# Kernel optimization log

Hardware: AMD Instinct MI355X
Metric: run time of the kernel (lower is better)

The kernel has to match this reference:

```python
import jax, jax.numpy as jnp
import numpy as np

# Layer node counts: [n0, n1, n2, n3] for a 3-hop sampled subgraph
N_NODES = [524288, 65536, 8192, 1024]
DIMS = [100, 256, 256, 47]


def sage_conv(x_src, x_dst, src, dst, Wl, bl, Wr, n_dst):
    # PyG SAGEConv: lin_l(mean_agg(neighbors)) + lin_r(root)
    msg = x_src[src]                                        # [E, in]
    agg = jax.ops.segment_sum(msg, dst, num_segments=n_dst)  # [n_dst, in]
    cnt = jax.ops.segment_sum(jnp.ones((src.shape[0],), dtype=x_src.dtype), dst,
                              num_segments=n_dst)
    agg = agg / jnp.maximum(cnt, 1.0)[:, None]               # mean, 0-deg -> 0
    return agg @ Wl + bl + x_dst @ Wr


def setup_inputs() -> dict:
    key = jax.random.key(0)
    ks = jax.random.split(key, 20)
    inp = {"x": jax.random.normal(ks[0], (N_NODES[0], DIMS[0]), dtype=jnp.float32)}
    E = [655360, 81920, 10240]
    for i in range(3):
        inp[f"src{i}"] = jax.random.randint(ks[1 + 2 * i], (E[i],), 0, N_NODES[i])
        inp[f"dst{i}"] = jax.random.randint(ks[2 + 2 * i], (E[i],), 0, N_NODES[i + 1])
    for i in range(3):
        fin, fout = DIMS[i], DIMS[i + 1]
        inp[f"Wl{i}"] = jax.random.normal(ks[7 + 3 * i], (fin, fout), jnp.float32) * (1.0 / np.sqrt(fin))
        inp[f"bl{i}"] = jnp.zeros((fout,), jnp.float32)
        inp[f"Wr{i}"] = jax.random.normal(ks[8 + 3 * i], (fin, fout), jnp.float32) * (1.0 / np.sqrt(fin))
    return inp


def reference(x, src0, dst0, src1, dst1, src2, dst2,
              Wl0, bl0, Wr0, Wl1, bl1, Wr1, Wl2, bl2, Wr2):
    srcs = [src0, src1, src2]
    dsts = [dst0, dst1, dst2]
    Wls = [Wl0, Wl1, Wl2]
    bls = [bl0, bl1, bl2]
    Wrs = [Wr0, Wr1, Wr2]
    h = x
    for i in range(3):
        n_dst = N_NODES[i + 1]
        h_dst = h[:n_dst]
        h = sage_conv(h, h_dst, srcs[i], dsts[i], Wls[i], bls[i], Wrs[i], n_dst)
        if i != 2:
            h = jax.nn.relu(h)  # dropout is identity in eval mode
    return jax.nn.log_softmax(h, axis=-1)
```

## Files before the change

### kernel.cpp

```cpp
#include <hip/hip_runtime.h>
#include <math.h>

constexpr int NN1 = 65536, NN2 = 8192, NN3 = 1024;
constexpr int E0 = 655360, E1 = 81920, E2 = 10240;
constexpr int ETOT = E0 + E1 + E2;
constexpr int NTOT = NN1 + NN2 + NN3;

static inline int cdiv(int a, int b) { return (a + b - 1) / b; }

typedef __bf16 bf16x8_t __attribute__((ext_vector_type(8)));
typedef float f32x4_t __attribute__((ext_vector_type(4)));

__device__ __forceinline__ unsigned short f2bf(float f) {
    union { float f; unsigned int u; } v; v.f = f;
    unsigned int r = v.u + 0x7fffu + ((v.u >> 16) & 1u);
    return (unsigned short)(r >> 16);
}
__device__ __forceinline__ float bf2f(unsigned short h) {
    union { unsigned int u; float f; } v; v.u = ((unsigned int)h) << 16;
    return v.f;
}

__global__ void count_all(const int* __restrict__ dst0, const int* __restrict__ dst1,
                          const int* __restrict__ dst2, int* __restrict__ cnt) {
    int i = blockIdx.x * 256 + threadIdx.x;
    if (i < E0) atomicAdd(&cnt[dst0[i]], 1);
    else if (i < E0 + E1) atomicAdd(&cnt[NN1 + dst1[i - E0]], 1);
    else if (i < ETOT) atomicAdd(&cnt[NN1 + NN2 + dst2[i - E0 - E1]], 1);
}

__global__ __launch_bounds__(1024) void scan1(const int* __restrict__ cnt, int n,
                                              int* __restrict__ ofs, int* __restrict__ sums) {
    __shared__ int s[1024];
    int i = blockIdx.x * 1024 + threadIdx.x;
    int v = (i < n) ? cnt[i] : 0;
    s[threadIdx.x] = v;
    __syncthreads();
    for (int off = 1; off < 1024; off <<= 1) {
        int t = (threadIdx.x >= off) ? s[threadIdx.x - off] : 0;
        __syncthreads();
        s[threadIdx.x] += t;
        __syncthreads();
    }
    if (i < n) ofs[i] = s[threadIdx.x] - v;
    if (threadIdx.x == 1023) sums[blockIdx.x] = s[1023];
}

__global__ void scan3(const int* __restrict__ sums, int n,
                      int* __restrict__ ofs, int* __restrict__ cursor) {
    __shared__ int pref_s;
    int c = (blockIdx.x * 256) >> 10;
    if (threadIdx.x < 64) {
        int v = 0;
        for (int j = threadIdx.x; j < c; j += 64) v += sums[j];
        for (int o = 32; o; o >>= 1) v += __shfl_down(v, o);
        if (threadIdx.x == 0) pref_s = v;
    }
    __syncthreads();
    int i = blockIdx.x * 256 + threadIdx.x;
    if (i < n) {
        int v = ofs[i] + pref_s;
        ofs[i] = v;
        cursor[i] = v;
    }
    if (blockIdx.x == 0 && threadIdx.x == 0) ofs[n] = ETOT;
}

__global__ void scatter_all(const int* __restrict__ src0, const int* __restrict__ dst0,
                            const int* __restrict__ src1, const int* __restrict__ dst1,
                            const int* __restrict__ src2, const int* __restrict__ dst2,
                            int* __restrict__ cursor, int* __restrict__ perm) {
    int i = blockIdx.x * 256 + threadIdx.x;
    if (i < E0) {
        int p = atomicAdd(&cursor[dst0[i]], 1);
        perm[p] = src0[i];
    } else if (i < E0 + E1) {
        int j = i - E0;
        int p = atomicAdd(&cursor[NN1 + dst1[j]], 1);
        perm[p] = src1[j];
    } else if (i < ETOT) {
        int j = i - E0 - E1;
        int p = atomicAdd(&cursor[NN1 + NN2 + dst2[j]], 1);
        perm[p] = src2[j];
    }
}

__global__ void prep_w(const float* __restrict__ Wl0, const float* __restrict__ Wr0,
                       unsigned short* __restrict__ Wt0a, unsigned short* __restrict__ Wt0b,
                       const float* __restrict__ Wl1, const float* __restrict__ Wr1,
                       unsigned short* __restrict__ Wt1a, unsigned short* __restrict__ Wt1b) {
    int b = blockIdx.x, t = threadIdx.x;
    if (b < 128) {
        int idx = b * 256 + t; int n = idx >> 7, k = idx & 127;
        Wt0a[idx] = f2bf(k < 100 ? Wl0[k * 256 + n] : 0.f);
    } else if (b < 256) {
        int idx = (b - 128) * 256 + t; int n = idx >> 7, k = idx & 127;
        Wt0b[idx] = f2bf(k < 100 ? Wr0[k * 256 + n] : 0.f);
    } else if (b < 512) {
        int idx = (b - 256) * 256 + t; int n = idx >> 8, k = idx & 255;
        Wt1a[idx] = f2bf(Wl1[k * 256 + n]);
    } else {
        int idx = (b - 512) * 256 + t; int n = idx >> 8, k = idx & 255;
        Wt1b[idx] = f2bf(Wr1[k * 256 + n]);
    }
}

__global__ __launch_bounds__(512) void fused_l0(const float* __restrict__ x,
                                                const int* __restrict__ perm,
                                                const int* __restrict__ ofs,
                                                const unsigned short* __restrict__ Wt0a,
                                                const unsigned short* __restrict__ Wt0b,
                                                const float* __restrict__ bias,
                                                unsigned short* __restrict__ h1) {
    __shared__ unsigned short As[128][136];
    __shared__ unsigned short Bs[256][40];
    int tid = threadIdx.x;
    int lane = tid & 63, wid = tid >> 6;
    int bm = blockIdx.x * 128;

    {
        int g = lane >> 5, l5 = lane & 31;
        bool act = l5 < 25;
        for (int r = 0; r < 16; ++r) {
            int row = wid * 16 + r;
            int node = bm + row;
            int s0 = ofs[node], s1 = ofs[node + 1];
            float inv = 1.0f / fmaxf((float)(s1 - s0), 1.0f);
            f32x4_t A0 = {0.f, 0.f, 0.f, 0.f}, A1 = A0, A2 = A0, A3 = A0;
            int e = s0;
            for (; e + 8 <= s1; e += 8) {
                int p0 = perm[e + 0 + g];
                int p1 = perm[e + 2 + g];
                int p2 = perm[e + 4 + g];
                int p3 = perm[e + 6 + g];
                if (act) {
                    A0 += *reinterpret_cast<const f32x4_t*>(x + (size_t)p0 * 100 + l5 * 4);
                    A1 += *reinterpret_cast<const f32x4_t*>(x + (size_t)p1 * 100 + l5 * 4);
                    A2 += *reinterpret_cast<const f32x4_t*>(x + (size_t)p2 * 100 + l5 * 4);
                    A3 += *reinterpret_cast<const f32x4_t*>(x + (size_t)p3 * 100 + l5 * 4);
                }
            }
            for (; e < s1; e += 2) {
                int idx = e + g;
                if (idx < s1 && act)
                    A0 += *reinterpret_cast<const f32x4_t*>(x + (size_t)perm[idx] * 100 + l5 * 4);
            }
            f32x4_t a = (A0 + A1) + (A2 + A3);
#pragma unroll
            for (int c = 0; c < 4; c++) a[c] += __shfl_xor(a[c], 32);
            if (lane < 25) {
                ushort4 o;
                o.x = f2bf(a[0] * inv); o.y = f2bf(a[1] * inv);
                o.z = f2bf(a[2] * inv); o.w = f2bf(a[3] * inv);
                *reinterpret_cast<ushort4*>(&As[row][lane * 4]) = o;
            } else if (lane < 32) {
                *reinterpret_cast<ushort4*>(&As[row][100 + (lane - 25) * 4]) = make_ushort4(0, 0, 0, 0);
            }
        }
    }

    f32x4_t acc[4][4];
#pragma unroll
    for (int i = 0; i < 4; i++)
#pragma unroll
        for (int j = 0; j < 4; j++)
#pragma unroll
            for (int r = 0; r < 4; r++) acc[i][j][r] = 0.f;

    int r0 = lane & 15, kg = lane >> 4;
    int wm = (wid >> 2) * 64, wn = (wid & 3) * 64;

    for (int pass = 0; pass < 2; ++pass) {
        const unsigned short* W = pass ? Wt0b : Wt0a;
        if (pass) {
            __syncthreads();
            int rown = tid >> 2, q = tid & 3;
            for (int c4 = q; c4 < 25; c4 += 4) {
                f32x4_t v = *reinterpret_cast<const f32x4_t*>(x + (size_t)(bm + rown) * 100 + c4 * 4);
                ushort4 o;
                o.x = f2bf(v[0]); o.y = f2bf(v[1]); o.z = f2bf(v[2]); o.w = f2bf(v[3]);
                *reinterpret_cast<ushort4*>(&As[rown][c4 * 4]) = o;
            }
            if (q == 3) {
#pragma unroll
                for (int c4 = 25; c4 < 32; ++c4)
                    *reinterpret_cast<ushort4*>(&As[rown][c4 * 4]) = make_ushort4(0, 0, 0, 0);
            }
        }
        for (int ks = 0; ks < 4; ++ks) {
            __syncthreads();
            for (int c = tid; c < 1024; c += 512) {
                int n = c >> 2, k8 = (c & 3) << 3;
                *reinterpret_cast<int4*>(&Bs[n][k8]) =
                    *reinterpret_cast<const int4*>(&W[(size_t)n * 128 + ks * 32 + k8]);
            }
            __syncthreads();
            bf16x8_t af[4], bfv[4];
#pragma unroll
            for (int mi = 0; mi < 4; mi++)
                af[mi] = *reinterpret_cast<const bf16x8_t*>(&As[wm + mi * 16 + r0][ks * 32 + kg * 8]);
#pragma unroll
            for (int ni = 0; ni < 4; ni++)
                bfv[ni] = *reinterpret_cast<const bf16x8_t*>(&Bs[wn + ni * 16 + r0][kg * 8]);
#pragma unroll
            for (int mi = 0; mi < 4; mi++)
#pragma unroll
                for (int ni = 0; ni < 4; ni++)
                    acc[mi][ni] = __builtin_amdgcn_mfma_f32_16x16x32_bf16(af[mi], bfv[ni], acc[mi][ni], 0, 0, 0);
        }
    }

    int cc = lane & 15, rr = (lane >> 4) * 4;
#pragma unroll
    for (int mi = 0; mi < 4; mi++) {
#pragma unroll
        for (int ni = 0; ni < 4; ni++) {
            int col = wn + ni * 16 + cc;
            float b = bias[col];
#pragma unroll
            for (int j = 0; j < 4; j++) {
                int row = bm + wm + mi * 16 + rr + j;
                float v = fmaxf(acc[mi][ni][j] + b, 0.f);
                h1[(size_t)row * 256 + col] = f2bf(v);
            }
        }
    }
}

__global__ __launch_bounds__(512) void fused_l1(const unsigned short* __restrict__ h1,
                                                const int* __restrict__ perm,
                                                const int* __restrict__ ofs,
                                                const unsigned short* __restrict__ Wt1a,
                                                const unsigned short* __restrict__ Wt1b,
                                                const float* __restrict__ bias,
                                                float* __restrict__ h2) {
    __shared__ unsigned short As[64][264];
    __shared__ unsigned short Bs[128][40];
    int tid = threadIdx.x;
    int lane = tid & 63, wid = tid >> 6;
    int bm = blockIdx.y * 64, bn = blockIdx.x * 128;

    for (int r = 0; r < 8; ++r) {
        int row = wid * 8 + r;
        int node = bm + row;
        int s0 = ofs[node], s1 = ofs[node + 1];
        float inv = 1.0f / fmaxf((float)(s1 - s0), 1.0f);
        float ac[4][4] = {};
        int e = s0;
        for (; e + 4 <= s1; e += 4) {
            ushort4 v[4];
#pragma unroll
            for (int u = 0; u < 4; u++)
                v[u] = *reinterpret_cast<const ushort4*>(h1 + (size_t)perm[e + u] * 256 + lane * 4);
#pragma unroll
            for (int u = 0; u < 4; u++) {
                ac[u][0] += bf2f(v[u].x); ac[u][1] += bf2f(v[u].y);
                ac[u][2] += bf2f(v[u].z); ac[u][3] += bf2f(v[u].w);
            }
        }
        for (; e < s1; e++) {
            ushort4 v = *reinterpret_cast<const ushort4*>(h1 + (size_t)perm[e] * 256 + lane * 4);
            ac[0][0] += bf2f(v.x); ac[0][1] += bf2f(v.y);
            ac[0][2] += bf2f(v.z); ac[0][3] += bf2f(v.w);
        }
        ushort4 o;
        o.x = f2bf((ac[0][0] + ac[1][0] + ac[2][0] + ac[3][0]) * inv);
        o.y = f2bf((ac[0][1] + ac[1][1] + ac[2][1] + ac[3][1]) * inv);
        o.z = f2bf((ac[0][2] + ac[1][2] + ac[2][2] + ac[3][2]) * inv);
        o.w = f2bf((ac[0][3] + ac[1][3] + ac[2][3] + ac[3][3]) * inv);
        *reinterpret_cast<ushort4*>(&As[row][lane * 4]) = o;
    }

    f32x4_t acc[2][2];
#pragma unroll
    for (int i = 0; i < 2; i++)
#pragma unroll
        for (int j = 0; j < 2; j++)
#pragma unroll
            for (int r = 0; r < 4; r++) acc[i][j][r] = 0.f;

    int r0 = lane & 15, kg = lane >> 4;
    int wm = (wid >> 2) * 32, wn = (wid & 3) * 32;

    for (int pass = 0; pass < 2; ++pass) {
        const unsigned short* W = pass ? Wt1b : Wt1a;
        if (pass) {
            __syncthreads();
            for (int c = tid; c < 2048; c += 512) {
                int row = c >> 5, k8 = (c & 31) << 3;
                *reinterpret_cast<int4*>(&As[row][k8]) =
                    *reinterpret_cast<const int4*>(&h1[(size_t)(bm + row) * 256 + k8]);
            }
        }
        for (int ks = 0; ks < 8; ++ks) {
            __syncthreads();
            {
                int c = tid;
                int n = c >> 2, k8 = (c & 3) << 3;
                *reinterpret_cast<int4*>(&Bs[n][k8]) =
                    *reinterpret_cast<const int4*>(&W[(size_t)(bn + n) * 256 + ks * 32 + k8]);
            }
            __syncthreads();
            bf16x8_t af[2], bfv[2];
#pragma unroll
            for (int mi = 0; mi < 2; mi++)
                af[mi] = *reinterpret_cast<const bf16x8_t*>(&As[wm + mi * 16 + r0][ks * 32 + kg * 8]);
#pragma unroll
            for (int ni = 0; ni < 2; ni++)
                bfv[ni] = *reinterpret_cast<const bf16x8_t*>(&Bs[wn + ni * 16 + r0][kg * 8]);
#pragma unroll
            for (int mi = 0; mi < 2; mi++)
#pragma unroll
                for (int ni = 0; ni < 2; ni++)
                    acc[mi][ni] = __builtin_amdgcn_mfma_f32_16x16x32_bf16(af[mi], bfv[ni], acc[mi][ni], 0, 0, 0);
        }
    }

    int cc = lane & 15, rr = (lane >> 4) * 4;
#pragma unroll
    for (int mi = 0; mi < 2; mi++) {
#pragma unroll
        for (int ni = 0; ni < 2; ni++) {
            int col = bn + wn + ni * 16 + cc;
            float b = bias[col];
#pragma unroll
            for (int j = 0; j < 4; j++) {
                int row = bm + wm + mi * 16 + rr + j;
                h2[(size_t)row * 256 + col] = fmaxf(acc[mi][ni][j] + b, 0.f);
            }
        }
    }
}

__global__ void agg_vec4_256(const float* __restrict__ x, const int* __restrict__ perm,
                             const int* __restrict__ ofs, float* __restrict__ agg, int nrows) {
    int wave = (blockIdx.x * blockDim.x + threadIdx.x) >> 6;
    int lane = threadIdx.x & 63;
    if (wave >= nrows) return;
    int s0 = ofs[wave], s1 = ofs[wave + 1];
    float4 acc = make_float4(0.f, 0.f, 0.f, 0.f);
    for (int e = s0; e < s1; e++) {
        const float4* xr = (const float4*)(x + (size_t)perm[e] * 256);
        float4 v = xr[lane];
        acc.x += v.x; acc.y += v.y; acc.z += v.z; acc.w += v.w;
    }
    float inv = 1.0f / fmaxf((float)(s1 - s0), 1.0f);
    acc.x *= inv; acc.y *= inv; acc.z *= inv; acc.w *= inv;
    ((float4*)(agg + (size_t)wave * 256))[lane] = acc;
}

__global__ __launch_bounds__(256) void gemm2_fused(const float* __restrict__ A1, const float* __restrict__ W1, int K1,
                                                   const float* __restrict__ A2, const float* __restrict__ W2, int K2,
                                                   const float* __restrict__ bias, float* __restrict__ out,
                                                   int M, int N) {
    __shared__ float As[16][65];
    __shared__ float Bs[16][64];
    int tid = threadIdx.x;
    int tx = tid & 15, ty = tid >> 4;
    int bm = blockIdx.y * 64;
    float acc[4][4] = {};
    for (int pass = 0; pass < 2; ++pass) {
        const float* A = pass ? A2 : A1;
        const float* W = pass ? W2 : W1;
        int K = pass ? K2 : K1;
        for (int k0 = 0; k0 < K; k0 += 16) {
#pragma unroll
            for (int i = 0; i < 4; i++) {
                int L = i * 256 + tid;
                int m = L >> 4, k = L & 15;
                int gm = bm + m, gk = k0 + k;
                float v = 0.f;
                if (gm < M && gk < K) v = A[(size_t)gm * K + gk];
                As[k][m] = v;
            }
#pragma unroll
            for (int i = 0; i < 4; i++) {
                int L = i * 256 + tid;
                int n = L & 63, k = L >> 6;
                int gk = k0 + k;
                float v = 0.f;
                if (gk < K && n < N) v = W[(size_t)gk * N + n];
                Bs[k][n] = v;
            }
            __syncthreads();
#pragma unroll
            for (int k = 0; k < 16; k++) {
                float a[4], b[4];
#pragma unroll
                for (int i = 0; i < 4; i++) a[i] = As[k][ty * 4 + i];
#pragma unroll
                for (int j = 0; j < 4; j++) b[j] = Bs[k][tx * 4 + j];
#pragma unroll
                for (int i = 0; i < 4; i++)
#pragma unroll
                    for (int j = 0; j < 4; j++) acc[i][j] += a[i] * b[j];
            }
            __syncthreads();
        }
    }
#pragma unroll
    for (int i = 0; i < 4; i++) {
        int gm = bm + ty * 4 + i;
        float vals[4];
        float vmax = -1e30f;
#pragma unroll
        for (int j = 0; j < 4; j++) {
            int gn = tx * 4 + j;
            vals[j] = (gn < N) ? acc[i][j] + bias[gn] : -1e30f;
            vmax = fmaxf(vmax, vals[j]);
        }
#pragma unroll
        for (int o = 1; o < 16; o <<= 1) vmax = fmaxf(vmax, __shfl_xor(vmax, o));
        float se = 0.f;
#pragma unroll
        for (int j = 0; j < 4; j++) {
            int gn = tx * 4 + j;
            if (gn < N) se += expf(vals[j] - vmax);
        }
#pragma unroll
        for (int o = 1; o < 16; o <<= 1) se += __shfl_xor(se, o);
        float ls = logf(se);
#pragma unroll
        for (int j = 0; j < 4; j++) {
            int gn = tx * 4 + j;
            if (gn < N && gm < M) out[(size_t)gm * N + gn] = vals[j] - vmax - ls;
        }
    }
}

extern "C" void kernel_launch(void* const* d_in, const int* in_sizes, int n_in,
                              void* d_out, int out_size, void* d_ws, size_t ws_size,
                              hipStream_t stream) {
    const float* x   = (const float*)d_in[0];
    const int* src0  = (const int*)d_in[1];
    const int* dst0  = (const int*)d_in[2];
    const int* src1  = (const int*)d_in[3];
    const int* dst1  = (const int*)d_in[4];
    const int* src2  = (const int*)d_in[5];
    const int* dst2  = (const int*)d_in[6];
    const float* Wl0 = (const float*)d_in[7];
    const float* bl0 = (const float*)d_in[8];
    const float* Wr0 = (const float*)d_in[9];
    const float* Wl1 = (const float*)d_in[10];
    const float* bl1 = (const float*)d_in[11];
    const float* Wr1 = (const float*)d_in[12];
    const float* Wl2 = (const float*)d_in[13];
    const float* bl2 = (const float*)d_in[14];
    const float* Wr2 = (const float*)d_in[15];
    float* out = (float*)d_out;

    char* p = (char*)d_ws;
    auto alloc = [&](size_t bytes) { char* r = p; p += (bytes + 255) & ~(size_t)255; return r; };
    unsigned short* h1   = (unsigned short*)alloc((size_t)NN1 * 256 * 2);
    float* h2    = (float*)alloc((size_t)NN2 * 256 * 4);
    float* agg2  = (float*)alloc((size_t)NN3 * 256 * 4);
    unsigned short* Wt0a = (unsigned short*)alloc(256 * 128 * 2);
    unsigned short* Wt0b = (unsigned short*)alloc(256 * 128 * 2);
    unsigned short* Wt1a = (unsigned short*)alloc(256 * 256 * 2);
    unsigned short* Wt1b = (unsigned short*)alloc(256 * 256 * 2);
    int* cnt    = (int*)alloc((size_t)NTOT * 4);
    int* ofs    = (int*)alloc((size_t)(NTOT + 1) * 4);
    int* cursor = (int*)alloc((size_t)(NTOT + 1) * 4);
    int* sums   = (int*)alloc(128 * 4);
    int* perm   = (int*)alloc((size_t)ETOT * 4);

    prep_w<<<768, 256, 0, stream>>>(Wl0, Wr0, Wt0a, Wt0b, Wl1, Wr1, Wt1a, Wt1b);
    hipMemsetAsync(cnt, 0, (size_t)NTOT * 4, stream);
    count_all<<<cdiv(ETOT, 256), 256, 0, stream>>>(dst0, dst1, dst2, cnt);
    int nb = cdiv(NTOT, 1024);
    scan1<<<nb, 1024, 0, stream>>>(cnt, NTOT, ofs, sums);
    scan3<<<cdiv(NTOT, 256), 256, 0, stream>>>(sums, NTOT, ofs, cursor);
    scatter_all<<<cdiv(ETOT, 256), 256, 0, stream>>>(src0, dst0, src1, dst1, src2, dst2, cursor, perm);

    fused_l0<<<NN1 / 128, 512, 0, stream>>>(x, perm, ofs, Wt0a, Wt0b, bl0, h1);

    {
        dim3 grid(2, NN2 / 64);
        fused_l1<<<grid, 512, 0, stream>>>(h1, perm, ofs + NN1, Wt1a, Wt1b, bl1, h2);
    }

    agg_vec4_256<<<cdiv(NN3 * 64, 256), 256, 0, stream>>>(h2, perm, ofs + NN1 + NN2, agg2, NN3);
    {
        dim3 grid(1, cdiv(NN3, 64));
        gemm2_fused<<<grid, 256, 0, stream>>>(agg2, Wl2, 256, h2, Wr2, 256, bl2, out, NN3, 47);
    }
}
```

Baseline: 291.4 us.

## Fuse weight prep into count, prefetch neighbor indices via shuffles, fuse layer-2 aggregation into GEMM

Merges the weight-transpose kernel into the degree-count kernel and folds the layer-2 mean aggregation into the final GEMM, removing two launches and the agg2 buffer. In the aggregation loops, each wave now loads its row offsets and up to 64 neighbor indices once, then broadcasts them with shuffles instead of issuing repeated scalar loads. It also adds occupancy hints to launch_bounds on the layer-0 and layer-1 kernels. The fused layer-2 kernel now gathers with only 16 blocks, so its parallelism is low, and the occupancy hint may force register spills.

```diff
diff --git a/kernel.cpp b/kernel.cpp
--- a/kernel.cpp
+++ b/kernel.cpp
@@ -21,12 +21,35 @@
     return v.f;
 }
 
-__global__ void count_all(const int* __restrict__ dst0, const int* __restrict__ dst1,
-                          const int* __restrict__ dst2, int* __restrict__ cnt) {
-    int i = blockIdx.x * 256 + threadIdx.x;
-    if (i < E0) atomicAdd(&cnt[dst0[i]], 1);
-    else if (i < E0 + E1) atomicAdd(&cnt[NN1 + dst1[i - E0]], 1);
-    else if (i < ETOT) atomicAdd(&cnt[NN1 + NN2 + dst2[i - E0 - E1]], 1);
+constexpr int CB = (ETOT + 255) / 256;
+__global__ void count_prep(const int* __restrict__ dst0, const int* __restrict__ dst1,
+                           const int* __restrict__ dst2, int* __restrict__ cnt,
+                           const float* __restrict__ Wl0, const float* __restrict__ Wr0,
+                           unsigned short* __restrict__ Wt0a, unsigned short* __restrict__ Wt0b,
+                           const float* __restrict__ Wl1, const float* __restrict__ Wr1,
+                           unsigned short* __restrict__ Wt1a, unsigned short* __restrict__ Wt1b) {
+    int b = blockIdx.x, t = threadIdx.x;
+    if (b < CB) {
+        int i = b * 256 + t;
+        if (i < E0) atomicAdd(&cnt[dst0[i]], 1);
+        else if (i < E0 + E1) atomicAdd(&cnt[NN1 + dst1[i - E0]], 1);
+        else if (i < ETOT) atomicAdd(&cnt[NN1 + NN2 + dst2[i - E0 - E1]], 1);
+        return;
+    }
+    b -= CB;
+    if (b < 128) {
+        int idx = b * 256 + t; int n = idx >> 7, k = idx & 127;
+        Wt0a[idx] = f2bf(k < 100 ? Wl0[k * 256 + n] : 0.f);
+    } else if (b < 256) {
+        int idx = (b - 128) * 256 + t; int n = idx >> 7, k = idx & 127;
+        Wt0b[idx] = f2bf(k < 100 ? Wr0[k * 256 + n] : 0.f);
+    } else if (b < 512) {
+        int idx = (b - 256) * 256 + t; int n = idx >> 8, k = idx & 255;
+        Wt1a[idx] = f2bf(Wl1[k * 256 + n]);
+    } else {
+        int idx = (b - 512) * 256 + t; int n = idx >> 8, k = idx & 255;
+        Wt1b[idx] = f2bf(Wr1[k * 256 + n]);
+    }
 }
 
 __global__ __launch_bounds__(1024) void scan1(const int* __restrict__ cnt, int n,
@@ -85,33 +108,13 @@
     }
 }
 
-__global__ void prep_w(const float* __restrict__ Wl0, const float* __restrict__ Wr0,
-                       unsigned short* __restrict__ Wt0a, unsigned short* __restrict__ Wt0b,
-                       const float* __restrict__ Wl1, const float* __restrict__ Wr1,
-                       unsigned short* __restrict__ Wt1a, unsigned short* __restrict__ Wt1b) {
-    int b = blockIdx.x, t = threadIdx.x;
-    if (b < 128) {
-        int idx = b * 256 + t; int n = idx >> 7, k = idx & 127;
-        Wt0a[idx] = f2bf(k < 100 ? Wl0[k * 256 + n] : 0.f);
-    } else if (b < 256) {
-        int idx = (b - 128) * 256 + t; int n = idx >> 7, k = idx & 127;
-        Wt0b[idx] = f2bf(k < 100 ? Wr0[k * 256 + n] : 0.f);
-    } else if (b < 512) {
-        int idx = (b - 256) * 256 + t; int n = idx >> 8, k = idx & 255;
-        Wt1a[idx] = f2bf(Wl1[k * 256 + n]);
-    } else {
-        int idx = (b - 512) * 256 + t; int n = idx >> 8, k = idx & 255;
-        Wt1b[idx] = f2bf(Wr1[k * 256 + n]);
-    }
-}
-
-__global__ __launch_bounds__(512) void fused_l0(const float* __restrict__ x,
-                                                const int* __restrict__ perm,
-                                                const int* __restrict__ ofs,
-                                                const unsigned short* __restrict__ Wt0a,
-                                                const unsigned short* __restrict__ Wt0b,
-                                                const float* __restrict__ bias,
-                                                unsigned short* __restrict__ h1) {
+__global__ __launch_bounds__(512, 4) void fused_l0(const float* __restrict__ x,
+                                                   const int* __restrict__ perm,
+                                                   const int* __restrict__ ofs,
+                                                   const unsigned short* __restrict__ Wt0a,
+                                                   const unsigned short* __restrict__ Wt0b,
+                                                   const float* __restrict__ bias,
+                                                   unsigned short* __restrict__ h1) {
     __shared__ unsigned short As[128][136];
     __shared__ unsigned short Bs[256][40];
     int tid = threadIdx.x;
@@ -121,28 +124,30 @@
     {
         int g = lane >> 5, l5 = lane & 31;
         bool act = l5 < 25;
+        int node0 = bm + wid * 16;
+        int myofs = (lane < 17) ? ofs[node0 + lane] : 0;
         for (int r = 0; r < 16; ++r) {
             int row = wid * 16 + r;
-            int node = bm + row;
-            int s0 = ofs[node], s1 = ofs[node + 1];
-            float inv = 1.0f / fmaxf((float)(s1 - s0), 1.0f);
+            int s0 = __shfl(myofs, r), s1 = __shfl(myofs, r + 1);
+            int deg = s1 - s0;
+            float inv = 1.0f / fmaxf((float)deg, 1.0f);
+            int dcap = min(deg, 64);
+            int pe = (lane < dcap) ? perm[s0 + lane] : 0;
             f32x4_t A0 = {0.f, 0.f, 0.f, 0.f}, A1 = A0, A2 = A0, A3 = A0;
-            int e = s0;
-            for (; e + 8 <= s1; e += 8) {
-                int p0 = perm[e + 0 + g];
-                int p1 = perm[e + 2 + g];
-                int p2 = perm[e + 4 + g];
-                int p3 = perm[e + 6 + g];
-                if (act) {
-                    A0 += *reinterpret_cast<const f32x4_t*>(x + (size_t)p0 * 100 + l5 * 4);
-                    A1 += *reinterpret_cast<const f32x4_t*>(x + (size_t)p1 * 100 + l5 * 4);
-                    A2 += *reinterpret_cast<const f32x4_t*>(x + (size_t)p2 * 100 + l5 * 4);
-                    A3 += *reinterpret_cast<const f32x4_t*>(x + (size_t)p3 * 100 + l5 * 4);
-                }
-            }
-            for (; e < s1; e += 2) {
+            for (int b = 0; b < dcap; b += 8) {
+                int e0 = b + g, e1 = b + 2 + g, e2 = b + 4 + g, e3 = b + 6 + g;
+                int p0 = __shfl(pe, e0), p1 = __shfl(pe, e1);
+                int p2 = __shfl(pe, e2), p3 = __shfl(pe, e3);
+                f32x4_t v0 = {0.f, 0.f, 0.f, 0.f}, v1 = v0, v2 = v0, v3 = v0;
+                if (act && e0 < dcap) v0 = *reinterpret_cast<const f32x4_t*>(x + (size_t)p0 * 100 + l5 * 4);
+                if (act && e1 < dcap) v1 = *reinterpret_cast<const f32x4_t*>(x + (size_t)p1 * 100 + l5 * 4);
+                if (act && e2 < dcap) v2 = *reinterpret_cast<const f32x4_t*>(x + (size_t)p2 * 100 + l5 * 4);
+                if (act && e3 < dcap) v3 = *reinterpret_cast<const f32x4_t*>(x + (size_t)p3 * 100 + l5 * 4);
+                A0 += v0; A1 += v1; A2 += v2; A3 += v3;
+            }
+            for (int e = s0 + 64; e < s1; e += 2) {
                 int idx = e + g;
-                if (idx < s1 && act)
+                if (act && idx < s1)
                     A0 += *reinterpret_cast<const f32x4_t*>(x + (size_t)perm[idx] * 100 + l5 * 4);
             }
             f32x4_t a = (A0 + A1) + (A2 + A3);
@@ -227,48 +232,53 @@
     }
 }
 
-__global__ __launch_bounds__(512) void fused_l1(const unsigned short* __restrict__ h1,
-                                                const int* __restrict__ perm,
-                                                const int* __restrict__ ofs,
-                                                const unsigned short* __restrict__ Wt1a,
-                                                const unsigned short* __restrict__ Wt1b,
-                                                const float* __restrict__ bias,
-                                                float* __restrict__ h2) {
+__global__ __launch_bounds__(512, 4) void fused_l1(const unsigned short* __restrict__ h1,
+                                                   const int* __restrict__ perm,
+                                                   const int* __restrict__ ofs,
+                                                   const unsigned short* __restrict__ Wt1a,
+                                                   const unsigned short* __restrict__ Wt1b,
+                                                   const float* __restrict__ bias,
+                                                   float* __restrict__ h2) {
     __shared__ unsigned short As[64][264];
     __shared__ unsigned short Bs[128][40];
     int tid = threadIdx.x;
     int lane = tid & 63, wid = tid >> 6;
     int bm = blockIdx.y * 64, bn = blockIdx.x * 128;
 
-    for (int r = 0; r < 8; ++r) {
-        int row = wid * 8 + r;
-        int node = bm + row;
-        int s0 = ofs[node], s1 = ofs[node + 1];
-        float inv = 1.0f / fmaxf((float)(s1 - s0), 1.0f);
-        float ac[4][4] = {};
-        int e = s0;
-        for (; e + 4 <= s1; e += 4) {
-            ushort4 v[4];
-#pragma unroll
-            for (int u = 0; u < 4; u++)
-                v[u] = *reinterpret_cast<const ushort4*>(h1 + (size_t)perm[e + u] * 256 + lane * 4);
-#pragma unroll
-            for (int u = 0; u < 4; u++) {
-                ac[u][0] += bf2f(v[u].x); ac[u][1] += bf2f(v[u].y);
-                ac[u][2] += bf2f(v[u].z); ac[u][3] += bf2f(v[u].w);
-            }
-        }
-        for (; e < s1; e++) {
-            ushort4 v = *reinterpret_cast<const ushort4*>(h1 + (size_t)perm[e] * 256 + lane * 4);
-            ac[0][0] += bf2f(v.x); ac[0][1] += bf2f(v.y);
-            ac[0][2] += bf2f(v.z); ac[0][3] += bf2f(v.w);
-        }
-        ushort4 o;
-        o.x = f2bf((ac[0][0] + ac[1][0] + ac[2][0] + ac[3][0]) * inv);
-        o.y = f2bf((ac[0][1] + ac[1][1] + ac[2][1] + ac[3][1]) * inv);
-        o.z = f2bf((ac[0][2] + ac[1][2] + ac[2][2] + ac[3][2]) * inv);
-        o.w = f2bf((ac[0][3] + ac[1][3] + ac[2][3] + ac[3][3]) * inv);
-        *reinterpret_cast<ushort4*>(&As[row][lane * 4]) = o;
+    {
+        int node0 = bm + wid * 8;
+        int myofs = (lane < 9) ? ofs[node0 + lane] : 0;
+        for (int r = 0; r < 8; ++r) {
+            int row = wid * 8 + r;
+            int s0 = __shfl(myofs, r), s1 = __shfl(myofs, r + 1);
+            int deg = s1 - s0;
+            float inv = 1.0f / fmaxf((float)deg, 1.0f);
+            int dcap = min(deg, 64);
+            int pe = (lane < dcap) ? perm[s0 + lane] : 0;
+            float ac[4][4] = {};
+            for (int b = 0; b < dcap; b += 4) {
+#pragma unroll
+                for (int u = 0; u < 4; u++) {
+                    int pu = __shfl(pe, b + u);
+                    ushort4 v = make_ushort4(0, 0, 0, 0);
+                    if (b + u < dcap)
+                        v = *reinterpret_cast<const ushort4*>(h1 + (size_t)pu * 256 + lane * 4);
+                    ac[u][0] += bf2f(v.x); ac[u][1] += bf2f(v.y);
+                    ac[u][2] += bf2f(v.z); ac[u][3] += bf2f(v.w);
+                }
+            }
+            for (int e = s0 + 64; e < s1; e++) {
+                ushort4 v = *reinterpret_cast<const ushort4*>(h1 + (size_t)perm[e] * 256 + lane * 4);
+                ac[0][0] += bf2f(v.x); ac[0][1] += bf2f(v.y);
+                ac[0][2] += bf2f(v.z); ac[0][3] += bf2f(v.w);
+            }
+            ushort4 o;
+            o.x = f2bf((ac[0][0] + ac[1][0] + ac[2][0] + ac[3][0]) * inv);
+            o.y = f2bf((ac[0][1] + ac[1][1] + ac[2][1] + ac[3][1]) * inv);
+            o.z = f2bf((ac[0][2] + ac[1][2] + ac[2][2] + ac[3][2]) * inv);
+            o.w = f2bf((ac[0][3] + ac[1][3] + ac[2][3] + ac[3][3]) * inv);
+            *reinterpret_cast<ushort4*>(&As[row][lane * 4]) = o;
+        }
     }
 
     f32x4_t acc[2][2];
@@ -332,54 +342,69 @@
     }
 }
 
-__global__ void agg_vec4_256(const float* __restrict__ x, const int* __restrict__ perm,
-                             const int* __restrict__ ofs, float* __restrict__ agg, int nrows) {
-    int wave = (blockIdx.x * blockDim.x + threadIdx.x) >> 6;
-    int lane = threadIdx.x & 63;
-    if (wave >= nrows) return;
-    int s0 = ofs[wave], s1 = ofs[wave + 1];
-    float4 acc = make_float4(0.f, 0.f, 0.f, 0.f);
-    for (int e = s0; e < s1; e++) {
-        const float4* xr = (const float4*)(x + (size_t)perm[e] * 256);
-        float4 v = xr[lane];
-        acc.x += v.x; acc.y += v.y; acc.z += v.z; acc.w += v.w;
-    }
-    float inv = 1.0f / fmaxf((float)(s1 - s0), 1.0f);
-    acc.x *= inv; acc.y *= inv; acc.z *= inv; acc.w *= inv;
-    ((float4*)(agg + (size_t)wave * 256))[lane] = acc;
-}
-
-__global__ __launch_bounds__(256) void gemm2_fused(const float* __restrict__ A1, const float* __restrict__ W1, int K1,
-                                                   const float* __restrict__ A2, const float* __restrict__ W2, int K2,
-                                                   const float* __restrict__ bias, float* __restrict__ out,
-                                                   int M, int N) {
+__global__ __launch_bounds__(256) void gemm2_all(const float* __restrict__ h2,
+                                                 const int* __restrict__ perm,
+                                                 const int* __restrict__ ofs,
+                                                 const float* __restrict__ W1,
+                                                 const float* __restrict__ W2,
+                                                 const float* __restrict__ bias,
+                                                 float* __restrict__ out,
+                                                 int M, int N) {
+    __shared__ float Agg[64][260];
     __shared__ float As[16][65];
     __shared__ float Bs[16][64];
     int tid = threadIdx.x;
+    int lane = tid & 63, wid = tid >> 6;
+    int bm = blockIdx.y * 64;
+
+    {
+        int node0 = bm + wid * 16;
+        int myofs = (lane < 17) ? ofs[node0 + lane] : 0;
+        for (int r = 0; r < 16; ++r) {
+            int row = wid * 16 + r;
+            int s0 = __shfl(myofs, r), s1 = __shfl(myofs, r + 1);
+            int deg = s1 - s0;
+            float inv = 1.0f / fmaxf((float)deg, 1.0f);
+            int dcap = min(deg, 64);
+            int pe = (lane < dcap) ? perm[s0 + lane] : 0;
+            f32x4_t B0 = {0.f, 0.f, 0.f, 0.f}, B1 = B0, B2 = B0, B3 = B0;
+            for (int b = 0; b < dcap; b += 4) {
+                int p0 = __shfl(pe, b), p1 = __shfl(pe, b + 1);
+                int p2 = __shfl(pe, b + 2), p3 = __shfl(pe, b + 3);
+                f32x4_t v0 = {0.f, 0.f, 0.f, 0.f}, v1 = v0, v2 = v0, v3 = v0;
+                if (b < dcap)     v0 = *reinterpret_cast<const f32x4_t*>(h2 + (size_t)p0 * 256 + lane * 4);
+                if (b + 1 < dcap) v1 = *reinterpret_cast<const f32x4_t*>(h2 + (size_t)p1 * 256 + lane * 4);
+                if (b + 2 < dcap) v2 = *reinterpret_cast<const f32x4_t*>(h2 + (size_t)p2 * 256 + lane * 4);
+                if (b + 3 < dcap) v3 = *reinterpret_cast<const f32x4_t*>(h2 + (size_t)p3 * 256 + lane * 4);
+                B0 += v0; B1 += v1; B2 += v2; B3 += v3;
+            }
+            for (int e = s0 + 64; e < s1; e++)
+                B0 += *reinterpret_cast<const f32x4_t*>(h2 + (size_t)perm[e] * 256 + lane * 4);
+            f32x4_t a = (B0 + B1) + (B2 + B3);
+#pragma unroll
+            for (int c = 0; c < 4; c++) Agg[row][lane * 4 + c] = a[c] * inv;
+        }
+    }
+    __syncthreads();
+
     int tx = tid & 15, ty = tid >> 4;
-    int bm = blockIdx.y * 64;
     float acc[4][4] = {};
     for (int pass = 0; pass < 2; ++pass) {
-        const float* A = pass ? A2 : A1;
         const float* W = pass ? W2 : W1;
-        int K = pass ? K2 : K1;
-        for (int k0 = 0; k0 < K; k0 += 16) {
+        for (int k0 = 0; k0 < 256; k0 += 16) {
+            __syncthreads();
 #pragma unroll
             for (int i = 0; i < 4; i++) {
                 int L = i * 256 + tid;
                 int m = L >> 4, k = L & 15;
-                int gm = bm + m, gk = k0 + k;
-                float v = 0.f;
-                if (gm < M && gk < K) v = A[(size_t)gm * K + gk];
-                As[k][m] = v;
+                As[k][m] = pass ? h2[(size_t)(bm + m) * 256 + k0 + k] : Agg[m][k0 + k];
             }
 #pragma unroll
             for (int i = 0; i < 4; i++) {
                 int L = i * 256 + tid;
                 int n = L & 63, k = L >> 6;
-                int gk = k0 + k;
                 float v = 0.f;
-                if (gk < K && n < N) v = W[(size_t)gk * N + n];
+                if (n < N) v = W[(size_t)(k0 + k) * N + n];
                 Bs[k][n] = v;
             }
             __syncthreads();
@@ -395,7 +420,6 @@
 #pragma unroll
                     for (int j = 0; j < 4; j++) acc[i][j] += a[i] * b[j];
             }
-            __syncthreads();
         }
     }
 #pragma unroll
@@ -453,7 +477,6 @@
     auto alloc = [&](size_t bytes) { char* r = p; p += (bytes + 255) & ~(size_t)255; return r; };
     unsigned short* h1   = (unsigned short*)alloc((size_t)NN1 * 256 * 2);
     float* h2    = (float*)alloc((size_t)NN2 * 256 * 4);
-    float* agg2  = (float*)alloc((size_t)NN3 * 256 * 4);
     unsigned short* Wt0a = (unsigned short*)alloc(256 * 128 * 2);
     unsigned short* Wt0b = (unsigned short*)alloc(256 * 128 * 2);
     unsigned short* Wt1a = (unsigned short*)alloc(256 * 256 * 2);
@@ -464,9 +487,9 @@
     int* sums   = (int*)alloc(128 * 4);
     int* perm   = (int*)alloc((size_t)ETOT * 4);
 
-    prep_w<<<768, 256, 0, stream>>>(Wl0, Wr0, Wt0a, Wt0b, Wl1, Wr1, Wt1a, Wt1b);
     hipMemsetAsync(cnt, 0, (size_t)NTOT * 4, stream);
-    count_all<<<cdiv(ETOT, 256), 256, 0, stream>>>(dst0, dst1, dst2, cnt);
+    count_prep<<<CB + 768, 256, 0, stream>>>(dst0, dst1, dst2, cnt,
+                                             Wl0, Wr0, Wt0a, Wt0b, Wl1, Wr1, Wt1a, Wt1b);
     int nb = cdiv(NTOT, 1024);
     scan1<<<nb, 1024, 0, stream>>>(cnt, NTOT, ofs, sums);
     scan3<<<cdiv(NTOT, 256), 256, 0, stream>>>(sums, NTOT, ofs, cursor);
@@ -479,9 +502,8 @@
         fused_l1<<<grid, 512, 0, stream>>>(h1, perm, ofs + NN1, Wt1a, Wt1b, bl1, h2);
     }
 
-    agg_vec4_256<<<cdiv(NN3 * 64, 256), 256, 0, stream>>>(h2, perm, ofs + NN1 + NN2, agg2, NN3);
     {
-        dim3 grid(1, cdiv(NN3, 64));
-        gemm2_fused<<<grid, 256, 0, stream>>>(agg2, Wl2, 256, h2, Wr2, 256, bl2, out, NN3, 47);
-    }
-}
+        dim3 grid(1, NN3 / 64);
+        gemm2_all<<<grid, 256, 0, stream>>>(h2, perm, ofs + NN1 + NN2, Wl2, Wr2, bl2, out, NN3, 47);
+    }
+}
```

Result: faster. 272.9 us (-6.3%).
